# Kernel optimization log

Measured on AMD Instinct MI355X. Metric: run time of the kernel, lower is better.

The kernel has to match this reference:

```python
import jax, jax.numpy as jnp
import numpy as np

STRIDE = 16
RATIOS = (0.5, 1.0, 2.0)
SCALES = (8, 16, 32)
NMS_THRESH = 0.7
NUM_PRE = 12000
NUM_POST = 2000
MIN_SIZE = 16.0


def _all_anchors(feat_h, feat_w):
    # base anchors centered at (stride/2, stride/2), (y1, x1, y2, x2)
    base = []
    for r in RATIOS:
        for s in SCALES:
            h = STRIDE * s * np.sqrt(r)
            w = STRIDE * s * np.sqrt(1.0 / r)
            c = STRIDE / 2.0
            base.append([c - h / 2.0, c - w / 2.0, c + h / 2.0, c + w / 2.0])
    base = np.asarray(base, np.float32)  # (A, 4)
    ys = np.arange(feat_h, dtype=np.float32) * STRIDE
    xs = np.arange(feat_w, dtype=np.float32) * STRIDE
    shift = np.stack(np.meshgrid(ys, xs, indexing='ij'), axis=-1)  # (H, W, 2) = (y, x)
    shift4 = np.concatenate([shift, shift], axis=-1)  # (H, W, 4)
    anchors = shift4[:, :, None, :] + base[None, None, :, :]  # (H, W, A, 4)
    return jnp.asarray(anchors.reshape(-1, 4))


def _conv(x, w, b, padding):
    y = jax.lax.conv_general_dilated(x, w, (1, 1), padding,
                                     dimension_numbers=('NCHW', 'OIHW', 'NCHW'))
    return y + b[None, :, None, None]


def _create_rpn_proposals(locs, scores, anchors, img_h, img_w):
    # box deparameterize (y1,x1,y2,x2 anchors; dy,dx,dh,dw locs)
    ha = anchors[:, 2] - anchors[:, 0]
    wa = anchors[:, 3] - anchors[:, 1]
    cya = anchors[:, 0] + 0.5 * ha
    cxa = anchors[:, 1] + 0.5 * wa
    cy = locs[:, 0] * ha + cya
    cx = locs[:, 1] * wa + cxa
    h = ha * jnp.exp(locs[:, 2])
    w = wa * jnp.exp(locs[:, 3])
    boxes = jnp.stack([cy - 0.5 * h, cx - 0.5 * w, cy + 0.5 * h, cx + 0.5 * w], axis=1)

    order = jnp.argsort(-scores)[:NUM_PRE]
    boxes = boxes[order]
    s = scores[order]

    lim = jnp.array([img_h, img_w, img_h, img_w], dtype=boxes.dtype)
    boxes = jnp.clip(boxes, 0.0, lim)
    valid = ((boxes[:, 2] - boxes[:, 0]) >= MIN_SIZE) & ((boxes[:, 3] - boxes[:, 1]) >= MIN_SIZE)

    areas = (boxes[:, 2] - boxes[:, 0]) * (boxes[:, 3] - boxes[:, 1])
    n = boxes.shape[0]
    idx = jnp.arange(n)

    def body(i, suppressed):
        bi = boxes[i]
        yy1 = jnp.maximum(bi[0], boxes[:, 0])
        xx1 = jnp.maximum(bi[1], boxes[:, 1])
        yy2 = jnp.minimum(bi[2], boxes[:, 2])
        xx2 = jnp.minimum(bi[3], boxes[:, 3])
        inter = jnp.maximum(yy2 - yy1, 0.0) * jnp.maximum(xx2 - xx1, 0.0)
        iou = inter / (areas[i] + areas - inter + 1e-10)
        new_sup = suppressed | ((iou > NMS_THRESH) & (idx > i))
        return jnp.where(suppressed[i], suppressed, new_sup)

    suppressed = jax.lax.fori_loop(0, n, body, ~valid)
    keep = (~suppressed) & valid
    rank = jnp.cumsum(keep) - 1
    tgt = jnp.where(keep & (rank < NUM_POST), rank, NUM_POST)  # overflow slot
    out = jnp.zeros((NUM_POST + 1, 4), boxes.dtype).at[tgt].set(boxes)[:NUM_POST]
    return out  # (2000, 4), zero-padded if fewer kept


def setup_inputs() -> dict:
    key = jax.random.key(0)
    ks = jax.random.split(key, 7)
    in_c, out_c, A = 1024, 512, 9
    x = jax.random.normal(ks[0], (1, in_c, 64, 64), dtype=jnp.float32)
    conv_w = jax.random.normal(ks[1], (out_c, in_c, 3, 3), jnp.float32) * 0.01
    conv_b = jnp.zeros((out_c,), jnp.float32)
    score_w = jax.random.normal(ks[2], (A * 2, out_c, 1, 1), jnp.float32) * 0.01
    score_b = jnp.zeros((A * 2,), jnp.float32)
    loc_w = jax.random.normal(ks[3], (A * 4, out_c, 1, 1), jnp.float32) * 0.01
    loc_b = jnp.zeros((A * 4,), jnp.float32)
    return {"x": x, "conv_w": conv_w, "conv_b": conv_b,
            "score_w": score_w, "score_b": score_b,
            "loc_w": loc_w, "loc_b": loc_b,
            "img_h": 1024, "img_w": 1024}


def reference(x, conv_w, conv_b, score_w, score_b, loc_w, loc_b, img_h, img_w):
    _, _, fh, fw = x.shape
    anchors = _all_anchors(fh, fw)  # (fh*fw*A, 4)
    h = jax.nn.leaky_relu(_conv(x, conv_w, conv_b, 'SAME'), 0.01)
    rpn_locs = _conv(h, loc_w, loc_b, 'VALID').transpose(0, 2, 3, 1).reshape(-1, 4)
    rpn_scores = _conv(h, score_w, score_b, 'VALID').transpose(0, 2, 3, 1).reshape(-1, 2)
    fg = jax.nn.softmax(rpn_scores, axis=1)[:, 1]
    rois = _create_rpn_proposals(jax.lax.stop_gradient(rpn_locs),
                                 jax.lax.stop_gradient(fg),
                                 anchors, img_h, img_w)
    return rpn_locs, rpn_scores, rois, anchors
```

## Files before the change

### kernel.cpp

```cpp
#include <hip/hip_runtime.h>
#include <cstdint>
#include <cstddef>
#include <math.h>

#define NANCH    36864
#define NPRE     12000
#define NPRE_PAD 12032
#define NW       188
#define SORT_N   16384
#define NPOST    2000

typedef double d4_t __attribute__((ext_vector_type(4)));

__device__ __forceinline__ int tribase(int ci) { return ci * NW - (ci * (ci - 1)) / 2; }

typedef __attribute__((address_space(1))) const void* as1cv_t;
typedef __attribute__((address_space(3))) void* as3v_t;
__device__ __forceinline__ void gload_lds16(const float* g, float* l)
{
    __builtin_amdgcn_global_load_lds((as1cv_t)g, (as3v_t)l, 16, 0, 0);
}

__global__ __launch_bounds__(256, 2)
void k_conv_mfma(const float* __restrict__ xg, const float* __restrict__ wg_,
                 const float* __restrict__ bg, float* __restrict__ hg)
{
    __shared__ __align__(16) float wlds[3][4608];
    __shared__ __align__(16) float xlds[3][1632];
    const int tid = threadIdx.x;
    const int oct = blockIdx.x & 7;
    const int y   = blockIdx.x >> 3;
    const int oc0 = oct << 6;
    const int l   = tid & 63;
    const int wv  = tid >> 6;
    const int g   = l >> 4;
    const int li  = l & 15;
    const int wm  = wv >> 1;
    const int wn  = wv & 1;
    const int slot5 = 16 + (wv & 1);

    int pr[4], qc[4];
    int aG = g;
    {
        d4_t Pz = {0., 0., 0., 0.}, Qz = {0., 0., 0., 0.}, Tz = {0., 0., 0., 0.};
        Pz = __builtin_amdgcn_mfma_f64_16x16x4f64((double)li, 1.0, Pz, 0, 0, 0);
        Qz = __builtin_amdgcn_mfma_f64_16x16x4f64(1.0, (double)li, Qz, 0, 0, 0);
        Tz = __builtin_amdgcn_mfma_f64_16x16x4f64((double)g, (double)(1 << (2 * g)),
                                                  Tz, 0, 0, 0);
        bool ok = true;
        const int tval = (int)Tz[0];
        if ((int)Tz[1] != tval || (int)Tz[2] != tval || (int)Tz[3] != tval) ok = false;
        int seen = 0;
#pragma unroll
        for (int j = 0; j < 4; ++j) {
            int d = (tval >> (2 * j)) & 3;
            seen |= 1 << d;
            if (d == g) aG = j;
        }
        if (seen != 15) ok = false;
#pragma unroll
        for (int r = 0; r < 4; ++r) {
            int pv = (int)Pz[r], qv = (int)Qz[r];
            if ((pv & 3) || (qv & 3)) ok = false;
            pr[r] = pv >> 2; qc[r] = qv >> 2;
            if (pr[r] > 15 || qc[r] > 15) ok = false;
        }
        if (!ok) {
#pragma unroll
            for (int r = 0; r < 4; ++r) { pr[r] = 4 * g + r; qc[r] = li; }
            aG = g;
        }
    }

    d4_t acc00 = {0., 0., 0., 0.}, acc01 = {0., 0., 0., 0.};
    d4_t acc10 = {0., 0., 0., 0.}, acc11 = {0., 0., 0., 0.};

    int xoff[7], loff[7];
#pragma unroll
    for (int t = 0; t < 7; ++t) {
        int f = tid + 256 * t;
        if (f < 1584) {
            int ic = f / 198; int r = f - ic * 198; int sr = r / 66; int gc = r - sr * 66;
            loff[t] = (ic * 3 + sr) * 68 + gc;
            int gy = y + sr - 1, gx = gc - 1;
            xoff[t] = (gy >= 0 && gy < 64 && gx >= 0 && gx < 64)
                      ? (ic * 4096 + gy * 64 + gx) : -1;
        } else { loff[t] = -1; xoff[t] = -1; }
    }
    int xoffL[7];
#pragma unroll
    for (int t = 0; t < 7; ++t) xoffL[t] = (xoff[t] >= 0) ? xoff[t] : 0;

    const float* wsrc0 = wg_ + (size_t)(oc0 + l) * 9216;
    const int abase = wm * 32 + li;
    const int bbase = (wn * 32 + li) * 4 + g;
    const int ax0   = (aG / 3) * 68 + (aG - 3 * (aG / 3)) + abase;
    float xr[7];
    float fa0, fa1, fb0, fb1;
    double pa0, pa1, pb0, pb1;

    {
#pragma unroll
        for (int i = 0; i < 4; ++i)
            gload_lds16(wsrc0 + 4 * (wv + 4 * i), &wlds[0][(wv + 4 * i) * 256]);
        gload_lds16(wsrc0 + 4 * slot5, &wlds[0][slot5 * 256]);
#pragma unroll
        for (int i = 0; i < 4; ++i)
            gload_lds16(wsrc0 + 72 + 4 * (wv + 4 * i), &wlds[1][(wv + 4 * i) * 256]);
        gload_lds16(wsrc0 + 72 + 4 * slot5, &wlds[1][slot5 * 256]);
#pragma unroll
        for (int t = 0; t < 7; ++t) xr[t] = xg[xoffL[t]];
#pragma unroll
        for (int t = 0; t < 7; ++t)
            if (loff[t] >= 0) xlds[0][loff[t]] = (xoff[t] >= 0) ? xr[t] : 0.f;
        {
            const float* xp = xg + 32768;
#pragma unroll
            for (int t = 0; t < 7; ++t) xr[t] = xp[xoffL[t]];
#pragma unroll
            for (int t = 0; t < 7; ++t)
                if (loff[t] >= 0) xlds[1][loff[t]] = (xoff[t] >= 0) ? xr[t] : 0.f;
        }
        {
            const float* xp = xg + 2 * 32768;
#pragma unroll
            for (int t = 0; t < 7; ++t) xr[t] = xp[xoffL[t]];
        }
        asm volatile("s_waitcnt lgkmcnt(0)" ::: "memory");
        asm volatile("s_waitcnt vmcnt(7)" ::: "memory");
        __builtin_amdgcn_s_barrier();
        fa0 = xlds[0][ax0]; fa1 = xlds[0][ax0 + 16];
        fb0 = wlds[0][bbase]; fb1 = wlds[0][bbase + 64];
        asm volatile("s_waitcnt lgkmcnt(0)" ::: "memory");
        pa0 = (double)fa0; pa1 = (double)fa1; pb0 = (double)fb0; pb1 = (double)fb1;
    }

#pragma unroll 1
    for (int cc = 0; cc < 128; ++cc) {
        int cb = cc % 3, nb = (cc + 1) % 3, sb = (cc + 2) % 3;
        if (cc + 2 < 128) {
            const float* wsrc = wsrc0 + (cc + 2) * 72;
            float* wdst = &wlds[sb][0];
#pragma unroll
            for (int i = 0; i < 4; ++i)
                gload_lds16(wsrc + 4 * (wv + 4 * i), wdst + (wv + 4 * i) * 256);
            gload_lds16(wsrc + 4 * slot5, wdst + slot5 * 256);
            float* xdst = &xlds[sb][0];
#pragma unroll
            for (int t = 0; t < 7; ++t)
                if (loff[t] >= 0) xdst[loff[t]] = (xoff[t] >= 0) ? xr[t] : 0.f;
            {
                int nc = (cc + 3 < 128) ? (cc + 3) : 127;
                const float* xp = xg + (size_t)nc * 32768;
#pragma unroll
                for (int t = 0; t < 7; ++t) xr[t] = xp[xoffL[t]];
            }
            asm volatile("s_waitcnt vmcnt(12)" ::: "memory");
        } else {
            asm volatile("s_waitcnt vmcnt(0)" ::: "memory");
        }
        __builtin_amdgcn_s_barrier();
        __builtin_amdgcn_sched_barrier(0);

        const float* wb = &wlds[cb][0];
        const float* xb = &xlds[cb][0];
        __builtin_amdgcn_s_setprio(1);
        acc00 = __builtin_amdgcn_mfma_f64_16x16x4f64(pa0, pb0, acc00, 0, 0, 0);
        acc01 = __builtin_amdgcn_mfma_f64_16x16x4f64(pa0, pb1, acc01, 0, 0, 0);
        acc10 = __builtin_amdgcn_mfma_f64_16x16x4f64(pa1, pb0, acc10, 0, 0, 0);
        acc11 = __builtin_amdgcn_mfma_f64_16x16x4f64(pa1, pb1, acc11, 0, 0, 0);
#pragma unroll
        for (int s = 1; s < 18; ++s) {
            int k   = 4 * s + aG;
            int icL = k / 9; int tap = k - 9 * icL;
            int ky  = tap / 3; int kx = tap - 3 * ky;
            int ax  = (icL * 3 + ky) * 68 + kx + abase;
            double a0 = (double)xb[ax];
            double a1 = (double)xb[ax + 16];
            double b0 = (double)wb[bbase + s * 256];
            double b1 = (double)wb[bbase + s * 256 + 64];
            acc00 = __builtin_amdgcn_mfma_f64_16x16x4f64(a0, b0, acc00, 0, 0, 0);
            acc01 = __builtin_amdgcn_mfma_f64_16x16x4f64(a0, b1, acc01, 0, 0, 0);
            acc10 = __builtin_amdgcn_mfma_f64_16x16x4f64(a1, b0, acc10, 0, 0, 0);
            acc11 = __builtin_amdgcn_mfma_f64_16x16x4f64(a1, b1, acc11, 0, 0, 0);
        }
        __builtin_amdgcn_s_setprio(0);
        __builtin_amdgcn_sched_barrier(0);

        if (cc < 127) {
            fa0 = xlds[nb][ax0]; fa1 = xlds[nb][ax0 + 16];
            fb0 = wlds[nb][bbase]; fb1 = wlds[nb][bbase + 64];
            asm volatile("s_waitcnt lgkmcnt(4)" ::: "memory");
            __builtin_amdgcn_s_barrier();
            asm volatile("s_waitcnt lgkmcnt(0)" ::: "memory");
            pa0 = (double)fa0; pa1 = (double)fa1; pb0 = (double)fb0; pb1 = (double)fb1;
        } else {
            asm volatile("s_waitcnt lgkmcnt(0)" ::: "memory");
            __builtin_amdgcn_s_barrier();
        }
    }

    __syncthreads();
    float* olds = &wlds[0][0];
    {
#pragma unroll
        for (int r = 0; r < 4; ++r) {
            const int oca = wn * 32 + qc[r];
            const int ocb = oca + 16;
            const double ba = (double)bg[oc0 + oca];
            const double bb = (double)bg[oc0 + ocb];
            const int pxa = wm * 32 + pr[r];
            const int pxb = pxa + 16;
            double t00 = acc00[r] + ba;
            double t01 = acc01[r] + bb;
            double t10 = acc10[r] + ba;
            double t11 = acc11[r] + bb;
            olds[oca * 68 + pxa] = (float)((t00 >= 0.0) ? t00 : 0.01 * t00);
            olds[ocb * 68 + pxa] = (float)((t01 >= 0.0) ? t01 : 0.01 * t01);
            olds[oca * 68 + pxb] = (float)((t10 >= 0.0) ? t10 : 0.01 * t10);
            olds[ocb * 68 + pxb] = (float)((t11 >= 0.0) ? t11 : 0.01 * t11);
        }
    }
    __syncthreads();
    {
        const int oc = tid >> 2, q = tid & 3;
        float* dst = hg + (size_t)(oc0 + oc) * 4096 + y * 64 + q * 16;
        const float* src = &olds[oc * 68 + q * 16];
#pragma unroll
        for (int j = 0; j < 4; ++j)
            *(float4*)(dst + 4 * j) = *(const float4*)(src + 4 * j);
    }
}

__global__ __launch_bounds__(256, 1)
void k_heads(const float* __restrict__ hg, const float* __restrict__ loc_w,
             const float* __restrict__ loc_b, const float* __restrict__ score_w,
             const float* __restrict__ score_b, const int* __restrict__ imh,
             const int* __restrict__ imw, float* __restrict__ out,
             float* __restrict__ boxes_all, unsigned long long* __restrict__ keys64)
{
    __shared__ float  hch[64 * 64];
    __shared__ float  wch[54 * 64];
    __shared__ float  ol[54 * 64];
    __shared__ double sld[18 * 64];
    const int y = blockIdx.x, tid = threadIdx.x;
    const int px = tid & 63, cg = tid >> 6;
    double acc[14];
#pragma unroll
    for (int u = 0; u < 14; ++u) acc[u] = 0.0;
    for (int cc = 0; cc < 8; ++cc) {
        __syncthreads();
#pragma unroll
        for (int t = 0; t < 16; ++t) {
            int f = tid + 256 * t;
            hch[f] = hg[(size_t)(cc * 64 + (f >> 6)) * 4096 + y * 64 + (f & 63)];
        }
#pragma unroll
        for (int t = 0; t < 14; ++t) {
            int f = tid + 256 * t;
            if (f < 54 * 64) {
                int ch = f >> 6, c = f & 63;
                wch[f] = (ch < 36) ? loc_w[ch * 512 + cc * 64 + c]
                                   : score_w[(ch - 36) * 512 + cc * 64 + c];
            }
        }
        __syncthreads();
        for (int c = 0; c < 64; ++c) {
            double hvd = (double)hch[c * 64 + px];
#pragma unroll
            for (int u = 0; u < 14; ++u) {
                int ch = cg + 4 * u;
                if (ch < 54) acc[u] = fma((double)wch[ch * 64 + c], hvd, acc[u]);
            }
        }
    }
    __syncthreads();
#pragma unroll
    for (int u = 0; u < 14; ++u) {
        int ch = cg + 4 * u;
        if (ch < 54) {
            double s = acc[u] + (double)((ch < 36) ? loc_b[ch] : score_b[ch - 36]);
            ol[ch * 64 + px] = (float)s;
            if (ch >= 36) sld[(ch - 36) * 64 + px] = s;
        }
    }
    __syncthreads();
    for (int f = tid; f < 64 * 36; f += 256) {
        int p = f / 36, ch = f - 36 * p;
        out[(size_t)(y * 64 + p) * 36 + ch] = ol[ch * 64 + p];
    }
    for (int f = tid; f < 64 * 18; f += 256) {
        int p = f / 18, ch = f - 18 * p;
        out[147456 + (size_t)(y * 64 + p) * 18 + ch] = ol[(36 + ch) * 64 + p];
    }
    const float fy = (float)(*imh), fx = (float)(*imw);
    float* anch = out + 229184;
    for (int t2 = tid; t2 < 576; t2 += 256) {
        int p = t2 / 9, a = t2 - 9 * p;
        int pg = y * 64 + p;
        int ar = a / 3, as = a - 3 * ar;
        double rr = (ar == 0) ? 0.5 : ((ar == 1) ? 1.0 : 2.0);
        double ss = (as == 0) ? 8.0 : ((as == 1) ? 16.0 : 32.0);
        double hh = 16.0 * ss * sqrt(rr), wwd = 16.0 * ss * sqrt(1.0 / rr);
        float by1 = (float)(8.0 - hh * 0.5), bx1 = (float)(8.0 - wwd * 0.5);
        float by2 = (float)(8.0 + hh * 0.5), bx2 = (float)(8.0 + wwd * 0.5);
        float sy = (float)(y * 16), sx = (float)(p * 16);
        float a0 = sy + by1, a1 = sx + bx1, a2 = sy + by2, a3 = sx + bx2;
        int base = (pg * 9 + a) * 4;
        anch[base + 0] = a0; anch[base + 1] = a1; anch[base + 2] = a2; anch[base + 3] = a3;
        double d = sld[(a * 2 + 1) * 64 + p] - sld[(a * 2) * 64 + p];
        long long bits = __double_as_longlong(d);
        unsigned long long u64 =
            (unsigned long long)(bits ^ ((bits >> 63) | (long long)0x8000000000000000LL));
        unsigned long long v = ~u64;
        keys64[pg * 9 + a] = (v & 0xFFFFFFFFFFFF0000ULL) | (unsigned long long)(pg * 9 + a);
        float dy = ol[(a * 4 + 0) * 64 + p], dxv = ol[(a * 4 + 1) * 64 + p];
        float dh = ol[(a * 4 + 2) * 64 + p], dwv = ol[(a * 4 + 3) * 64 + p];
        float hA = a2 - a0, wA = a3 - a1;
        float cya = a0 + 0.5f * hA, cxa = a1 + 0.5f * wA;
        float cy = dy * hA + cya, cx = dxv * wA + cxa;
        float hb = hA * expf(dh), wb = wA * expf(dwv);
        float b0 = fminf(fmaxf(cy - 0.5f * hb, 0.f), fy);
        float b1 = fminf(fmaxf(cx - 0.5f * wb, 0.f), fx);
        float b2 = fminf(fmaxf(cy + 0.5f * hb, 0.f), fy);
        float b3 = fminf(fmaxf(cx + 0.5f * wb, 0.f), fx);
        boxes_all[base + 0] = b0; boxes_all[base + 1] = b1;
        boxes_all[base + 2] = b2; boxes_all[base + 3] = b3;
    }
}

__global__ __launch_bounds__(1024, 1)
void k_select(const unsigned long long* __restrict__ keys64,
              const float* __restrict__ boxes_all,
              unsigned long long* __restrict__ sortbuf, float* __restrict__ sbox,
              float* __restrict__ areas, unsigned long long* __restrict__ suppr)
{
    __shared__ unsigned int hist[256];
    __shared__ unsigned int sh_below, sh_prefix, sh_nsel;
    __shared__ unsigned long long tile[4096];
    const int tid = threadIdx.x;
    if (tid == 0) { sh_below = 0; sh_prefix = 0; sh_nsel = 0; }
    __syncthreads();
    for (int p = 3; p >= 0; --p) {
        if (tid < 256) hist[tid] = 0;
        __syncthreads();
        unsigned int pref = sh_prefix;
        int shift = p * 8;
        for (int i = tid; i < NANCH; i += 1024) {
            unsigned int k = (unsigned int)(keys64[i] >> 32);
            bool match = (p == 3) || ((k >> (shift + 8)) == pref);
            if (match) atomicAdd(&hist[(k >> shift) & 255u], 1u);
        }
        __syncthreads();
        if (tid == 0) {
            unsigned int below = sh_below, cacc = 0;
            int b = 0;
            for (; b < 256; ++b) {
                if (below + cacc + hist[b] >= NPRE) break;
                cacc += hist[b];
            }
            if (b > 255) b = 255;
            sh_below = below + cacc;
            sh_prefix = (pref << 8) | (unsigned int)b;
        }
        __syncthreads();
    }
    const unsigned int P = sh_prefix;
    for (int i = tid; i < NANCH; i += 1024) {
        unsigned long long k = keys64[i];
        if ((unsigned int)(k >> 32) <= P) {
            unsigned int pos = atomicAdd(&sh_nsel, 1u);
            if (pos < SORT_N) sortbuf[pos] = k;
        }
    }
    __syncthreads();
    unsigned int nsel = sh_nsel; if (nsel > SORT_N) nsel = SORT_N;
    for (unsigned int i = nsel + tid; i < SORT_N; i += 1024) sortbuf[i] = ~0ULL;
    __syncthreads();
    for (int T = 0; T < 4; ++T) {
        for (int t = tid; t < 4096; t += 1024) tile[t] = sortbuf[T * 4096 + t];
        __syncthreads();
        for (int k2 = 2; k2 <= 4096; k2 <<= 1) {
            for (int j = k2 >> 1; j > 0; j >>= 1) {
                for (int t = tid; t < 2048; t += 1024) {
                    int i = ((t & ~(j - 1)) << 1) | (t & (j - 1));
                    int ip = i | j;
                    bool up = (((T * 4096 + i) & k2) == 0);
                    unsigned long long A = tile[i], B = tile[ip];
                    if ((A > B) == up) { tile[i] = B; tile[ip] = A; }
                }
                __syncthreads();
            }
        }
        for (int t = tid; t < 4096; t += 1024) sortbuf[T * 4096 + t] = tile[t];
        __syncthreads();
    }
    auto gstage = [&](int k2, int j) {
        for (int t = tid; t < 8192; t += 1024) {
            int i = ((t & ~(j - 1)) << 1) | (t & (j - 1));
            int ip = i | j;
            bool up = ((i & k2) == 0);
            unsigned long long A = sortbuf[i], B = sortbuf[ip];
            if ((A > B) == up) { sortbuf[i] = B; sortbuf[ip] = A; }
        }
        __syncthreads();
    };
    auto ltail = [&](int k2) {
        for (int T = 0; T < 4; ++T) {
            for (int t = tid; t < 4096; t += 1024) tile[t] = sortbuf[T * 4096 + t];
            __syncthreads();
            for (int j = 2048; j > 0; j >>= 1) {
                for (int t = tid; t < 2048; t += 1024) {
                    int i = ((t & ~(j - 1)) << 1) | (t & (j - 1));
                    int ip = i | j;
                    bool up = (((T * 4096 + i) & k2) == 0);
                    unsigned long long A = tile[i], B = tile[ip];
                    if ((A > B) == up) { tile[i] = B; tile[ip] = A; }
                }
                __syncthreads();
            }
            for (int t = tid; t < 4096; t += 1024) sortbuf[T * 4096 + t] = tile[t];
            __syncthreads();
        }
    };
    gstage(8192, 4096);  ltail(8192);
    gstage(16384, 8192); gstage(16384, 4096); ltail(16384);

    if (tid < NW) suppr[tid] = (tid == NW - 1) ? 0xFFFFFFFF00000000ULL : 0ULL;
    __syncthreads();
    for (int r = tid; r < NPRE_PAD; r += 1024) {
        float b0 = 0, b1 = 0, b2 = 0, b3 = 0;
        if (r < NPRE) {
            unsigned int idx = (unsigned int)(sortbuf[r] & 0xFFFFULL);
            const float* bp = boxes_all + (size_t)idx * 4;
            b0 = bp[0]; b1 = bp[1]; b2 = bp[2]; b3 = bp[3];
        }
        sbox[r * 4 + 0] = b0; sbox[r * 4 + 1] = b1;
        sbox[r * 4 + 2] = b2; sbox[r * 4 + 3] = b3;
        areas[r] = (b2 - b0) * (b3 - b1);
        if (r < NPRE) {
            bool valid = ((b2 - b0) >= 16.0f) && ((b3 - b1) >= 16.0f);
            if (!valid) atomicOr(&suppr[r >> 6], 1ULL << (r & 63));
        }
    }
}

__global__ __launch_bounds__(256, 1)
void k_mask(const float* __restrict__ sbox, const float* __restrict__ areas,
            unsigned long long* __restrict__ mask)
{
    const int cj = blockIdx.x, q = blockIdx.y;
    __shared__ float4 bx[64];
    __shared__ float aj[64];
    const int t = threadIdx.x;
    const int j0 = cj * 64;
    if (t < 64) { bx[t] = ((const float4*)sbox)[j0 + t]; aj[t] = areas[j0 + t]; }
    __syncthreads();
    const int c0 = ((cj + 1) * q) >> 2, c1 = ((cj + 1) * (q + 1)) >> 2;
    for (int i0 = c0 * 64; i0 < c1 * 64; i0 += 256) {
        int i = i0 + t;
        if (i < c1 * 64) {
            const float4 p = ((const float4*)sbox)[i];
            const float ai = areas[i];
            unsigned long long w = 0;
            for (int jj = 0; jj < 64; ++jj) {
                float4 qb = bx[jj];
                float yy1 = fmaxf(p.x, qb.x), xx1 = fmaxf(p.y, qb.y);
                float yy2 = fminf(p.z, qb.z), xx2 = fminf(p.w, qb.w);
                float inter = fmaxf(yy2 - yy1, 0.f) * fmaxf(xx2 - xx1, 0.f);
                float iou = inter / (ai + aj[jj] - inter + 1e-10f);
                w |= ((unsigned long long)((iou > 0.7f) && (j0 + jj > i))) << jj;
            }
            int ci = i >> 6;
            mask[(size_t)(tribase(ci) + (cj - ci)) * 64 + (i & 63)] = w;
        }
    }
}

__global__ __launch_bounds__(256, 1)
void k_scan(const unsigned long long* __restrict__ mask,
            const unsigned long long* __restrict__ suppr,
            const float* __restrict__ sbox, float* __restrict__ rois)
{
    __shared__ unsigned long long rvs[NW];
    __shared__ unsigned long long curw;
    __shared__ unsigned long long keptw[NW];
    __shared__ unsigned long long diagbuf[2][64];
    __shared__ int totkept, brk;
    __shared__ int pref[NW + 1];
    const int tid = threadIdx.x;
    if (tid < NW) { rvs[tid] = suppr[tid]; keptw[tid] = 0ULL; }
    if (tid == 0) { totkept = 0; brk = 0; }
    if (tid < 64) diagbuf[0][tid] = mask[tid];
    __syncthreads();
    for (int c = 0; c < NW; ++c) {
        unsigned long long pf = 0;
        const bool isPf = (tid >= 64 && tid < 128 && c + 1 < NW);
        if (isPf) pf = mask[((size_t)tribase(c + 1)) * 64 + (tid - 64)];
        if (tid < 64) {
            unsigned long long diag = diagbuf[c & 1][tid];
            unsigned long long w = rvs[c];
            for (int b = 0; b < 64; ++b) {
                unsigned long long db = __shfl(diag, b, 64);
                if (!((w >> b) & 1ULL)) w |= db;
            }
            if (tid == 0) {
                curw = w;
                keptw[c] = ~w;
                totkept += __popcll(~w);
                if (totkept >= NPOST) brk = 1;
            }
        }
        __syncthreads();
        if (brk) break;
        unsigned long long kw = ~curw;
        if (kw && tid > c && tid < NW) {
            const unsigned long long* mrow = mask + (size_t)(tribase(c) + (tid - c)) * 64;
            unsigned long long acc = 0;
            while (kw) {
                unsigned long long m0 = 0, m1 = 0, m2 = 0, m3 = 0,
                                   m4 = 0, m5 = 0, m6 = 0, m7 = 0;
                int b = (int)__builtin_ctzll(kw); m0 = mrow[b]; kw &= kw - 1;
                if (kw) { b = (int)__builtin_ctzll(kw); m1 = mrow[b]; kw &= kw - 1; }
                if (kw) { b = (int)__builtin_ctzll(kw); m2 = mrow[b]; kw &= kw - 1; }
                if (kw) { b = (int)__builtin_ctzll(kw); m3 = mrow[b]; kw &= kw - 1; }
                if (kw) { b = (int)__builtin_ctzll(kw); m4 = mrow[b]; kw &= kw - 1; }
                if (kw) { b = (int)__builtin_ctzll(kw); m5 = mrow[b]; kw &= kw - 1; }
                if (kw) { b = (int)__builtin_ctzll(kw); m6 = mrow[b]; kw &= kw - 1; }
                if (kw) { b = (int)__builtin_ctzll(kw); m7 = mrow[b]; kw &= kw - 1; }
                acc |= ((m0 | m1) | (m2 | m3)) | ((m4 | m5) | (m6 | m7));
            }
            rvs[tid] |= acc;
        }
        if (isPf) diagbuf[(c + 1) & 1][tid - 64] = pf;
        __syncthreads();
    }
    __syncthreads();
    if (tid == 0) {
        int s = 0;
        for (int c = 0; c < NW; ++c) { pref[c] = s; s += __popcll(keptw[c]); }
        pref[NW] = s;
    }
    __syncthreads();
    int total = pref[NW]; if (total > NPOST) total = NPOST;
    for (int r = total * 4 + tid; r < NPOST * 4; r += 256) rois[r] = 0.f;
    if (tid < NW) {
        unsigned long long kw = keptw[tid];
        int r = pref[tid];
        for (int b = 0; b < 64; ++b) {
            if ((kw >> b) & 1ULL) {
                if (r < NPOST) {
                    const float* bp = sbox + (size_t)(tid * 64 + b) * 4;
                    rois[r * 4 + 0] = bp[0]; rois[r * 4 + 1] = bp[1];
                    rois[r * 4 + 2] = bp[2]; rois[r * 4 + 3] = bp[3];
                }
                ++r;
            }
        }
    }
}

extern "C" void kernel_launch(void* const* d_in, const int* in_sizes, int n_in,
                              void* d_out, int out_size, void* d_ws, size_t ws_size,
                              hipStream_t stream)
{
    const float* x       = (const float*)d_in[0];
    const float* conv_w  = (const float*)d_in[1];
    const float* conv_b  = (const float*)d_in[2];
    const float* score_w = (const float*)d_in[3];
    const float* score_b = (const float*)d_in[4];
    const float* loc_w   = (const float*)d_in[5];
    const float* loc_b   = (const float*)d_in[6];
    const int*   imh     = (const int*)d_in[7];
    const int*   imw     = (const int*)d_in[8];
    float* out = (float*)d_out;
    char* ws = (char*)d_ws;
    float* h                    = (float*)(ws);
    float* boxes_all            = (float*)(ws + 8388608);
    unsigned long long* keys64  = (unsigned long long*)(ws + 8978432);
    float* sbox                 = (float*)(ws + 9273344);
    float* areas                = (float*)(ws + 9465856);
    unsigned long long* suppr   = (unsigned long long*)(ws + 9513984);
    unsigned long long* sortbuf = (unsigned long long*)(ws + 9515520);
    unsigned long long* mask    = (unsigned long long*)(ws + 9646592);

    k_conv_mfma<<<512, 256, 0, stream>>>(x, conv_w, conv_b, h);
    k_heads <<<64, 256, 0, stream>>>(h, loc_w, loc_b, score_w, score_b, imh, imw,
                                     out, boxes_all, keys64);
    k_select<<<1, 1024, 0, stream>>>(keys64, boxes_all, sortbuf, sbox, areas, suppr);
    k_mask  <<<dim3(188, 4), 256, 0, stream>>>(sbox, areas, mask);
    k_scan  <<<1, 256, 0, stream>>>(mask, suppr, sbox, out + 221184);
}
```

Before: 1.702 ms.

## Split conv input-channel reduction into four sequential launches with fp64 partial accumulators

The 3x3 conv kernel now runs as four template-phase launches, each covering 32 of the 128 input-channel chunks. Between launches the fp64 accumulators are written to and reloaded from a workspace buffer, and only the final phase applies bias and leaky-ReLU and writes h. The grid stays at 512 blocks per launch, so parallelism does not grow. This adds launch overhead, extra global traffic for the partial sums, and repeated prologue/pipeline fill, apparently to test or shorten per-launch duration.

```diff
diff --git a/kernel.cpp b/kernel.cpp
--- a/kernel.cpp
+++ b/kernel.cpp
@@ -21,10 +21,14 @@
     __builtin_amdgcn_global_load_lds((as1cv_t)g, (as3v_t)l, 16, 0, 0);
 }
 
+template<int PHASE>
 __global__ __launch_bounds__(256, 2)
 void k_conv_mfma(const float* __restrict__ xg, const float* __restrict__ wg_,
-                 const float* __restrict__ bg, float* __restrict__ hg)
+                 const float* __restrict__ bg, float* __restrict__ hg,
+                 double* __restrict__ Pg)
 {
+    constexpr int NCH = 32;
+    constexpr int CB  = PHASE * NCH;
     __shared__ __align__(16) float wlds[3][4608];
     __shared__ __align__(16) float xlds[3][1632];
     const int tid = threadIdx.x;
@@ -72,8 +76,22 @@
         }
     }
 
-    d4_t acc00 = {0., 0., 0., 0.}, acc01 = {0., 0., 0., 0.};
-    d4_t acc10 = {0., 0., 0., 0.}, acc11 = {0., 0., 0., 0.};
+    d4_t acc00, acc01, acc10, acc11;
+    double* Pb = Pg + (size_t)blockIdx.x * 4096;
+    if constexpr (PHASE > 0) {
+#pragma unroll
+        for (int r = 0; r < 4; ++r) {
+            acc00[r] = Pb[(r + 0) * 256 + tid];
+            acc01[r] = Pb[(r + 4) * 256 + tid];
+            acc10[r] = Pb[(r + 8) * 256 + tid];
+            acc11[r] = Pb[(r + 12) * 256 + tid];
+        }
+    } else {
+#pragma unroll
+        for (int r = 0; r < 4; ++r) {
+            acc00[r] = 0.0; acc01[r] = 0.0; acc10[r] = 0.0; acc11[r] = 0.0;
+        }
+    }
 
     int xoff[7], loff[7];
 #pragma unroll
@@ -91,7 +109,8 @@
 #pragma unroll
     for (int t = 0; t < 7; ++t) xoffL[t] = (xoff[t] >= 0) ? xoff[t] : 0;
 
-    const float* wsrc0 = wg_ + (size_t)(oc0 + l) * 9216;
+    const float* wsrc0 = wg_ + (size_t)(oc0 + l) * 9216 + CB * 72;
+    const float* xgp   = xg + (size_t)CB * 32768;
     const int abase = wm * 32 + li;
     const int bbase = (wn * 32 + li) * 4 + g;
     const int ax0   = (aG / 3) * 68 + (aG - 3 * (aG / 3)) + abase;
@@ -109,12 +128,12 @@
             gload_lds16(wsrc0 + 72 + 4 * (wv + 4 * i), &wlds[1][(wv + 4 * i) * 256]);
         gload_lds16(wsrc0 + 72 + 4 * slot5, &wlds[1][slot5 * 256]);
 #pragma unroll
-        for (int t = 0; t < 7; ++t) xr[t] = xg[xoffL[t]];
+        for (int t = 0; t < 7; ++t) xr[t] = xgp[xoffL[t]];
 #pragma unroll
         for (int t = 0; t < 7; ++t)
             if (loff[t] >= 0) xlds[0][loff[t]] = (xoff[t] >= 0) ? xr[t] : 0.f;
         {
-            const float* xp = xg + 32768;
+            const float* xp = xgp + 32768;
 #pragma unroll
             for (int t = 0; t < 7; ++t) xr[t] = xp[xoffL[t]];
 #pragma unroll
@@ -122,7 +141,7 @@
                 if (loff[t] >= 0) xlds[1][loff[t]] = (xoff[t] >= 0) ? xr[t] : 0.f;
         }
         {
-            const float* xp = xg + 2 * 32768;
+            const float* xp = xgp + 2 * 32768;
 #pragma unroll
             for (int t = 0; t < 7; ++t) xr[t] = xp[xoffL[t]];
         }
@@ -136,9 +155,9 @@
     }
 
 #pragma unroll 1
-    for (int cc = 0; cc < 128; ++cc) {
+    for (int cc = 0; cc < NCH; ++cc) {
         int cb = cc % 3, nb = (cc + 1) % 3, sb = (cc + 2) % 3;
-        if (cc + 2 < 128) {
+        if (cc + 2 < NCH) {
             const float* wsrc = wsrc0 + (cc + 2) * 72;
             float* wdst = &wlds[sb][0];
 #pragma unroll
@@ -150,8 +169,8 @@
             for (int t = 0; t < 7; ++t)
                 if (loff[t] >= 0) xdst[loff[t]] = (xoff[t] >= 0) ? xr[t] : 0.f;
             {
-                int nc = (cc + 3 < 128) ? (cc + 3) : 127;
-                const float* xp = xg + (size_t)nc * 32768;
+                int nc = (cc + 3 < NCH) ? (cc + 3) : (NCH - 1);
+                const float* xp = xgp + (size_t)nc * 32768;
 #pragma unroll
                 for (int t = 0; t < 7; ++t) xr[t] = xp[xoffL[t]];
             }
@@ -187,7 +206,7 @@
         __builtin_amdgcn_s_setprio(0);
         __builtin_amdgcn_sched_barrier(0);
 
-        if (cc < 127) {
+        if (cc < NCH - 1) {
             fa0 = xlds[nb][ax0]; fa1 = xlds[nb][ax0 + 16];
             fb0 = wlds[nb][bbase]; fb1 = wlds[nb][bbase + 64];
             asm volatile("s_waitcnt lgkmcnt(4)" ::: "memory");
@@ -200,35 +219,45 @@
         }
     }
 
-    __syncthreads();
-    float* olds = &wlds[0][0];
-    {
+    if constexpr (PHASE < 3) {
 #pragma unroll
         for (int r = 0; r < 4; ++r) {
-            const int oca = wn * 32 + qc[r];
-            const int ocb = oca + 16;
-            const double ba = (double)bg[oc0 + oca];
-            const double bb = (double)bg[oc0 + ocb];
-            const int pxa = wm * 32 + pr[r];
-            const int pxb = pxa + 16;
-            double t00 = acc00[r] + ba;
-            double t01 = acc01[r] + bb;
-            double t10 = acc10[r] + ba;
-            double t11 = acc11[r] + bb;
-            olds[oca * 68 + pxa] = (float)((t00 >= 0.0) ? t00 : 0.01 * t00);
-            olds[ocb * 68 + pxa] = (float)((t01 >= 0.0) ? t01 : 0.01 * t01);
-            olds[oca * 68 + pxb] = (float)((t10 >= 0.0) ? t10 : 0.01 * t10);
-            olds[ocb * 68 + pxb] = (float)((t11 >= 0.0) ? t11 : 0.01 * t11);
-        }
-    }
-    __syncthreads();
-    {
-        const int oc = tid >> 2, q = tid & 3;
-        float* dst = hg + (size_t)(oc0 + oc) * 4096 + y * 64 + q * 16;
-        const float* src = &olds[oc * 68 + q * 16];
-#pragma unroll
-        for (int j = 0; j < 4; ++j)
-            *(float4*)(dst + 4 * j) = *(const float4*)(src + 4 * j);
+            Pb[(r + 0) * 256 + tid]  = acc00[r];
+            Pb[(r + 4) * 256 + tid]  = acc01[r];
+            Pb[(r + 8) * 256 + tid]  = acc10[r];
+            Pb[(r + 12) * 256 + tid] = acc11[r];
+        }
+    } else {
+        __syncthreads();
+        float* olds = &wlds[0][0];
+        {
+#pragma unroll
+            for (int r = 0; r < 4; ++r) {
+                const int oca = wn * 32 + qc[r];
+                const int ocb = oca + 16;
+                const double ba = (double)bg[oc0 + oca];
+                const double bb = (double)bg[oc0 + ocb];
+                const int pxa = wm * 32 + pr[r];
+                const int pxb = pxa + 16;
+                double t00 = acc00[r] + ba;
+                double t01 = acc01[r] + bb;
+                double t10 = acc10[r] + ba;
+                double t11 = acc11[r] + bb;
+                olds[oca * 68 + pxa] = (float)((t00 >= 0.0) ? t00 : 0.01 * t00);
+                olds[ocb * 68 + pxa] = (float)((t01 >= 0.0) ? t01 : 0.01 * t01);
+                olds[oca * 68 + pxb] = (float)((t10 >= 0.0) ? t10 : 0.01 * t10);
+                olds[ocb * 68 + pxb] = (float)((t11 >= 0.0) ? t11 : 0.01 * t11);
+            }
+        }
+        __syncthreads();
+        {
+            const int oc = tid >> 2, q = tid & 3;
+            float* dst = hg + (size_t)(oc0 + oc) * 4096 + y * 64 + q * 16;
+            const float* src = &olds[oc * 68 + q * 16];
+#pragma unroll
+            for (int j = 0; j < 4; ++j)
+                *(float4*)(dst + 4 * j) = *(const float4*)(src + 4 * j);
+        }
     }
 }
 
@@ -583,8 +612,12 @@
     unsigned long long* suppr   = (unsigned long long*)(ws + 9513984);
     unsigned long long* sortbuf = (unsigned long long*)(ws + 9515520);
     unsigned long long* mask    = (unsigned long long*)(ws + 9646592);
-
-    k_conv_mfma<<<512, 256, 0, stream>>>(x, conv_w, conv_b, h);
+    double* Pacc                = (double*)(ws + 20971520);
+
+    k_conv_mfma<0><<<512, 256, 0, stream>>>(x, conv_w, conv_b, h, Pacc);
+    k_conv_mfma<1><<<512, 256, 0, stream>>>(x, conv_w, conv_b, h, Pacc);
+    k_conv_mfma<2><<<512, 256, 0, stream>>>(x, conv_w, conv_b, h, Pacc);
+    k_conv_mfma<3><<<512, 256, 0, stream>>>(x, conv_w, conv_b, h, Pacc);
     k_heads <<<64, 256, 0, stream>>>(h, loc_w, loc_b, score_w, score_b, imh, imw,
                                      out, boxes_all, keys64);
     k_select<<<1, 1024, 0, stream>>>(keys64, boxes_all, sortbuf, sbox, areas, suppr);
```

New measurement: 1.725 ms. No clear change (+1.3%).
